# Kernel optimization log

Measured on AMD Instinct MI355X. Metric: run time of the kernel, lower is better.

The kernel has to match this reference:

```python
import jax, jax.numpy as jnp
import numpy as np

B, N, D = 2, 2048, 1024          # batch, query tokens, model dim
NC, DC = 77, 768                 # context tokens, context dim (CLIP)
H, DH = 16, 64                   # heads, head dim (H*DH == D)
FF = 4 * D                       # GEGLU inner dim
SCALE = DH ** -0.5
EPS = 1e-5


def setup_inputs() -> dict:
    key = jax.random.key(0)
    ks = iter(jax.random.split(key, 32))
    rn = lambda *s: jax.random.normal(next(ks), s, dtype=jnp.float32) * 0.02
    inp = {
        'x': jax.random.normal(next(ks), (B, N, D), dtype=jnp.float32),
        'context': jax.random.normal(next(ks), (B, NC, DC), dtype=jnp.float32),
        # attn1 (self-attention): all projections from dim D
        'w1_q': rn(D, D), 'w1_k': rn(D, D), 'w1_v': rn(D, D),
        'w1_o': rn(D, D), 'b1_o': jnp.zeros((D,), jnp.float32),
        # attn2 (cross-attention): k/v from context dim DC
        'w2_q': rn(D, D), 'w2_k': rn(DC, D), 'w2_v': rn(DC, D),
        'w2_o': rn(D, D), 'b2_o': jnp.zeros((D,), jnp.float32),
        # layernorms
        'ln1_g': jnp.ones((D,), jnp.float32), 'ln1_b': jnp.zeros((D,), jnp.float32),
        'ln2_g': jnp.ones((D,), jnp.float32), 'ln2_b': jnp.zeros((D,), jnp.float32),
        'ln3_g': jnp.ones((D,), jnp.float32), 'ln3_b': jnp.zeros((D,), jnp.float32),
        # GEGLU feed-forward: proj -> 2*FF (value, gate), then FF -> D
        'ff_w1': rn(D, 2 * FF), 'ff_b1': jnp.zeros((2 * FF,), jnp.float32),
        'ff_w2': rn(FF, D), 'ff_b2': jnp.zeros((D,), jnp.float32),
    }
    return inp


def _layer_norm(x, g, b):
    mu = jnp.mean(x, axis=-1, keepdims=True)
    var = jnp.mean(jnp.square(x - mu), axis=-1, keepdims=True)
    return (x - mu) * jax.lax.rsqrt(var + EPS) * g + b


def _attention(xq, ctx, wq, wk, wv, wo, bo):
    b, n, _ = xq.shape
    m = ctx.shape[1]
    q = (xq @ wq).reshape(b, n, H, DH)
    k = (ctx @ wk).reshape(b, m, H, DH)
    v = (ctx @ wv).reshape(b, m, H, DH)
    sim = jnp.einsum('bihd,bjhd->bhij', q, k) * SCALE
    attn = jax.nn.softmax(sim, axis=-1)
    out = jnp.einsum('bhij,bjhd->bihd', attn, v).reshape(b, n, H * DH)
    return out @ wo + bo


def reference(x, context,
              w1_q, w1_k, w1_v, w1_o, b1_o,
              w2_q, w2_k, w2_v, w2_o, b2_o,
              ln1_g, ln1_b, ln2_g, ln2_b, ln3_g, ln3_b,
              ff_w1, ff_b1, ff_w2, ff_b2):
    # self-attention + residual
    h = _layer_norm(x, ln1_g, ln1_b)
    x = _attention(h, h, w1_q, w1_k, w1_v, w1_o, b1_o) + x
    # cross-attention + residual
    h = _layer_norm(x, ln2_g, ln2_b)
    x = _attention(h, context, w2_q, w2_k, w2_v, w2_o, b2_o) + x
    # GEGLU feed-forward + residual (torch F.gelu is exact erf)
    h = _layer_norm(x, ln3_g, ln3_b)
    p = h @ ff_w1 + ff_b1
    val, gate = p[..., :FF], p[..., FF:]
    x = (val * jax.nn.gelu(gate, approximate=False)) @ ff_w2 + ff_b2 + x
    return x
```

## Files before the change

kernel.cpp:

```cpp
#include <hip/hip_runtime.h>
#include <hip/hip_bf16.h>
#include <math.h>

#define B_    2
#define N_    2048
#define D_    1024
#define NC_   77
#define DC_   768
#define H_    16
#define DH_   64
#define FF_   4096
#define EPS_  1e-5f
#define SCALE_ 0.125f
#define NEG_BIG -1e30f

typedef __attribute__((ext_vector_type(8))) short short8;
typedef __attribute__((ext_vector_type(4))) float f32x4;
#define MFMA16(a, b, c) __builtin_amdgcn_mfma_f32_16x16x32_bf16(a, b, c, 0, 0, 0)

static __device__ __forceinline__ unsigned short f2bf_raw(float f) {
    union { float f; unsigned int i; } x; x.f = f;
    unsigned int r = x.i + 0x7fffu + ((x.i >> 16) & 1u);
    return (unsigned short)(r >> 16);
}

static __device__ __forceinline__ float erf_fast(float x) {
    const float ax = fabsf(x);
    const float t = __frcp_rn(fmaf(0.3275911f, ax, 1.0f));
    float p = fmaf(1.061405429f, t, -1.453152027f);
    p = fmaf(p, t, 1.421413741f);
    p = fmaf(p, t, -0.284496736f);
    p = fmaf(p, t, 0.254829592f);
    p = p * t;
    const float e = __expf(-ax * ax);
    float r = fmaf(-p, e, 1.0f);
    return copysignf(r, x);
}

static __device__ __forceinline__ void gload16(const void* g, void* l) {
    __builtin_amdgcn_global_load_lds(
        (const __attribute__((address_space(1))) void*)g,
        (__attribute__((address_space(3))) void*)l, 16, 0, 0);
}

__global__ __launch_bounds__(256) void wtrans_k(const float* __restrict__ src,
                                                unsigned short* __restrict__ dst,
                                                int K, int N) {
    __shared__ unsigned short t[64][68];
    const int k0 = blockIdx.y * 64, n0 = blockIdx.x * 64;
    const int rr = threadIdx.x >> 4;
    const int cc = (threadIdx.x & 15) * 4;
#pragma unroll
    for (int p = 0; p < 4; p++) {
        int k = rr + p * 16;
        float4 vd = *(const float4*)&src[(size_t)(k0 + k) * N + n0 + cc];
        t[k][cc + 0] = f2bf_raw(vd.x); t[k][cc + 1] = f2bf_raw(vd.y);
        t[k][cc + 2] = f2bf_raw(vd.z); t[k][cc + 3] = f2bf_raw(vd.w);
    }
    __syncthreads();
#pragma unroll
    for (int p = 0; p < 4; p++) {
        int n = rr + p * 16;
        ushort4 o;
        o.x = t[cc + 0][n]; o.y = t[cc + 1][n];
        o.z = t[cc + 2][n]; o.w = t[cc + 3][n];
        *(ushort4*)&dst[(size_t)(n0 + n) * K + k0 + cc] = o;
    }
}

struct WT6 { const float* s[6]; unsigned short* d[6]; };
__global__ __launch_bounds__(256) void wtrans6_k(WT6 p) {
    __shared__ unsigned short t[64][68];
    const float* __restrict__ src = p.s[blockIdx.z];
    unsigned short* __restrict__ dst = p.d[blockIdx.z];
    const int K = 1024, N = 1024;
    const int k0 = blockIdx.y * 64, n0 = blockIdx.x * 64;
    const int rr = threadIdx.x >> 4;
    const int cc = (threadIdx.x & 15) * 4;
#pragma unroll
    for (int pq = 0; pq < 4; pq++) {
        int k = rr + pq * 16;
        float4 vd = *(const float4*)&src[(size_t)(k0 + k) * N + n0 + cc];
        t[k][cc + 0] = f2bf_raw(vd.x); t[k][cc + 1] = f2bf_raw(vd.y);
        t[k][cc + 2] = f2bf_raw(vd.z); t[k][cc + 3] = f2bf_raw(vd.w);
    }
    __syncthreads();
#pragma unroll
    for (int pq = 0; pq < 4; pq++) {
        int n = rr + pq * 16;
        ushort4 o;
        o.x = t[cc + 0][n]; o.y = t[cc + 1][n];
        o.z = t[cc + 2][n]; o.w = t[cc + 3][n];
        *(ushort4*)&dst[(size_t)(n0 + n) * K + k0 + cc] = o;
    }
}

__global__ __launch_bounds__(256) void ln_k(const float* __restrict__ x,
                                            const float* __restrict__ g,
                                            const float* __restrict__ b,
                                            unsigned short* __restrict__ out) {
    int row = blockIdx.x;
    const float* xr = x + (size_t)row * D_;
    float v0[4]; float s = 0.f, sq = 0.f;
#pragma unroll
    for (int i = 0; i < 4; i++) {
        float t = xr[threadIdx.x + 256 * i];
        v0[i] = t; s += t; sq += t * t;
    }
#pragma unroll
    for (int off = 32; off; off >>= 1) {
        s  += __shfl_xor(s,  off);
        sq += __shfl_xor(sq, off);
    }
    __shared__ float rs[4], rq[4];
    int wave = threadIdx.x >> 6, lane = threadIdx.x & 63;
    if (lane == 0) { rs[wave] = s; rq[wave] = sq; }
    __syncthreads();
    s  = rs[0] + rs[1] + rs[2] + rs[3];
    sq = rq[0] + rq[1] + rq[2] + rq[3];
    float mu  = s * (1.f / D_);
    float var = sq * (1.f / D_) - mu * mu;
    float inv = rsqrtf(var + EPS_);
#pragma unroll
    for (int i = 0; i < 4; i++) {
        int c = threadIdx.x + 256 * i;
        out[(size_t)row * D_ + c] = f2bf_raw((v0[i] - mu) * inv * g[c] + b[c]);
    }
}

__global__ __launch_bounds__(256) void gemm_mfma_k(
        const unsigned short* __restrict__ A,
        const unsigned short* __restrict__ BT,
        const float* __restrict__ bias,
        const float* __restrict__ res,
        float* __restrict__ outf,
        unsigned short* __restrict__ oq,
        unsigned short* __restrict__ ok,
        unsigned short* __restrict__ ov,
        int M, int N, int K, int mode) {
    __shared__ unsigned short As[128 * 32];
    __shared__ unsigned short Bs[128 * 32];
    const int tid = threadIdx.x;
    const int w = tid >> 6, lane = tid & 63, quad = lane >> 4, l15 = lane & 15;
    const int wm = w >> 1, wn = w & 1;
    const int m0 = blockIdx.y * 128, n0 = blockIdx.x * 128;
    const int srow = lane >> 2;
    const int schunk = lane & 3;
    const int kswz = (schunk ^ (srow & 3)) * 8;
    const int rdsw = (quad ^ (l15 & 3)) * 8;

    const unsigned short* pA[2];
    const unsigned short* pB[2];
#pragma unroll
    for (int i = 0; i < 2; i++) {
        int r = (w * 2 + i) * 16;
        pA[i] = &A[(size_t)(m0 + r + srow) * K + kswz];
        pB[i] = &BT[(size_t)(n0 + r + srow) * K + kswz];
    }

    f32x4 acc[4][4] = {};
    for (int k0 = 0; k0 < K; k0 += 32) {
#pragma unroll
        for (int i = 0; i < 2; i++) {
            int r = (w * 2 + i) * 16;
            gload16(pA[i], &As[r * 32]);
            gload16(pB[i], &Bs[r * 32]);
            pA[i] += 32; pB[i] += 32;
        }
        __syncthreads();
        short8 af[4], bf[4];
#pragma unroll
        for (int i = 0; i < 4; i++) {
            af[i] = *(const short8*)&As[(wm * 64 + i * 16 + l15) * 32 + rdsw];
            bf[i] = *(const short8*)&Bs[(wn * 64 + i * 16 + l15) * 32 + rdsw];
        }
#pragma unroll
        for (int i = 0; i < 4; i++)
#pragma unroll
            for (int j = 0; j < 4; j++)
                acc[i][j] = MFMA16(af[i], bf[j], acc[i][j]);
        __syncthreads();
    }
#pragma unroll
    for (int i = 0; i < 4; i++) {
#pragma unroll
        for (int r = 0; r < 4; r++) {
            const int row = m0 + wm * 64 + i * 16 + quad * 4 + r;
#pragma unroll
            for (int j = 0; j < 4; j++) {
                const int col = n0 + wn * 64 + j * 16 + l15;
                float c = acc[i][j][r];
                if (mode == 0) {
                    int which = col >> 10, cc = col & 1023;
                    unsigned short* dst = which == 0 ? oq : (which == 1 ? ok : ov);
                    dst[(size_t)row * 1024 + cc] = f2bf_raw(which == 0 ? c * SCALE_ : c);
                } else {
                    outf[(size_t)row * N + col] =
                        c + bias[col] + res[(size_t)row * N + col];
                }
            }
        }
    }
}

__global__ __launch_bounds__(256) void gemm64_k(
        const unsigned short* __restrict__ A,
        const unsigned short* __restrict__ BT,
        const float* __restrict__ bias,
        const float* __restrict__ res,
        float* __restrict__ outf,
        unsigned short* __restrict__ outb,
        float scale,
        int M, int N, int K, int mode) {
    __shared__ unsigned short As[64 * 64];
    __shared__ unsigned short Bs[64 * 64];
    const int tid = threadIdx.x;
    const int w = tid >> 6, lane = tid & 63, quad = lane >> 4, l15 = lane & 15;
    const int wm = w >> 1, wn = w & 1;
    const int m0 = blockIdx.y * 64, n0 = blockIdx.x * 64;
    const int sr8 = lane >> 3;
    const int sc8 = lane & 7;

    const unsigned short* pA[2];
    const unsigned short* pB[2];
#pragma unroll
    for (int i = 0; i < 2; i++) {
        int row = w * 16 + i * 8 + sr8;
        int gch = sc8 ^ (row & 7);
        pA[i] = &A[(size_t)(m0 + row) * K + gch * 8];
        pB[i] = &BT[(size_t)(n0 + row) * K + gch * 8];
    }

    f32x4 acc[2][2] = {};
    for (int k0 = 0; k0 < K; k0 += 64) {
#pragma unroll
        for (int i = 0; i < 2; i++) {
            gload16(pA[i], &As[(w * 16 + i * 8) * 64]);
            gload16(pB[i], &Bs[(w * 16 + i * 8) * 64]);
            pA[i] += 64; pB[i] += 64;
        }
        __syncthreads();
        short8 af[2][2], bf[2][2];
#pragma unroll
        for (int ii = 0; ii < 2; ii++) {
            int ra = wm * 32 + ii * 16 + l15;
            int rb = wn * 32 + ii * 16 + l15;
#pragma unroll
            for (int kh = 0; kh < 2; kh++) {
                int ca = (kh * 4 + quad) ^ (ra & 7);
                int cb = (kh * 4 + quad) ^ (rb & 7);
                af[ii][kh] = *(const short8*)&As[ra * 64 + ca * 8];
                bf[ii][kh] = *(const short8*)&Bs[rb * 64 + cb * 8];
            }
        }
#pragma unroll
        for (int ii = 0; ii < 2; ii++)
#pragma unroll
            for (int jj = 0; jj < 2; jj++) {
                acc[ii][jj] = MFMA16(af[ii][0], bf[jj][0], acc[ii][jj]);
                acc[ii][jj] = MFMA16(af[ii][1], bf[jj][1], acc[ii][jj]);
            }
        __syncthreads();
    }
#pragma unroll
    for (int ii = 0; ii < 2; ii++) {
#pragma unroll
        for (int r = 0; r < 4; r++) {
            const int row = m0 + wm * 32 + ii * 16 + quad * 4 + r;
#pragma unroll
            for (int jj = 0; jj < 2; jj++) {
                const int col = n0 + wn * 32 + jj * 16 + l15;
                float c = acc[ii][jj][r];
                if (mode == 0) {
                    outb[(size_t)row * N + col] = f2bf_raw(c * scale);
                } else {
                    outf[(size_t)row * N + col] =
                        c + bias[col] + res[(size_t)row * N + col];
                }
            }
        }
    }
}

__global__ __launch_bounds__(256, 4) void geglu_mfma_k(
        const unsigned short* __restrict__ A,
        const unsigned short* __restrict__ BT,
        const float* __restrict__ bias,
        unsigned short* __restrict__ outg,
        int M, int K) {
    __shared__ unsigned short As[64 * 64];
    __shared__ unsigned short Bv[128 * 64];
    __shared__ unsigned short Bg[128 * 64];
    const int tid = threadIdx.x;
    const int w = tid >> 6, lane = tid & 63, quad = lane >> 4, l15 = lane & 15;
    const int m0 = blockIdx.y * 64, n0 = blockIdx.x * 128;
    const int sr8 = lane >> 3, sc8 = lane & 7;

    f32x4 accv[4][2] = {}, accg[4][2] = {};
    for (int k0 = 0; k0 < K; k0 += 64) {
#pragma unroll
        for (int i = 0; i < 2; i++) {
            int row = w * 16 + i * 8 + sr8;
            int gch = sc8 ^ (row & 7);
            gload16(&A[(size_t)(m0 + row) * K + k0 + gch * 8], &As[(w * 16 + i * 8) * 64]);
        }
#pragma unroll
        for (int i = 0; i < 4; i++) {
            int row = w * 32 + i * 8 + sr8;
            int gch = sc8 ^ (row & 7);
            gload16(&BT[(size_t)(n0 + row) * K + k0 + gch * 8], &Bv[(w * 32 + i * 8) * 64]);
            gload16(&BT[(size_t)(FF_ + n0 + row) * K + k0 + gch * 8], &Bg[(w * 32 + i * 8) * 64]);
        }
        __syncthreads();
        short8 af[4][2];
#pragma unroll
        for (int ii = 0; ii < 4; ii++) {
            int ra = ii * 16 + l15;
#pragma unroll
            for (int kh = 0; kh < 2; kh++) {
                int ca = (kh * 4 + quad) ^ (ra & 7);
                af[ii][kh] = *(const short8*)&As[ra * 64 + ca * 8];
            }
        }
#pragma unroll
        for (int jj = 0; jj < 2; jj++) {
            const int rb = w * 32 + jj * 16 + l15;
            const int c0 = (0 * 4 + quad) ^ (rb & 7);
            const int c1 = (1 * 4 + quad) ^ (rb & 7);
            const short8 bv0 = *(const short8*)&Bv[rb * 64 + c0 * 8];
            const short8 bv1 = *(const short8*)&Bv[rb * 64 + c1 * 8];
            const short8 bg0 = *(const short8*)&Bg[rb * 64 + c0 * 8];
            const short8 bg1 = *(const short8*)&Bg[rb * 64 + c1 * 8];
#pragma unroll
            for (int ii = 0; ii < 4; ii++) {
                accv[ii][jj] = MFMA16(af[ii][0], bv0, accv[ii][jj]);
                accv[ii][jj] = MFMA16(af[ii][1], bv1, accv[ii][jj]);
                accg[ii][jj] = MFMA16(af[ii][0], bg0, accg[ii][jj]);
                accg[ii][jj] = MFMA16(af[ii][1], bg1, accg[ii][jj]);
            }
        }
        __syncthreads();
    }
#pragma unroll
    for (int ii = 0; ii < 4; ii++) {
#pragma unroll
        for (int r = 0; r < 4; r++) {
            const int row = m0 + ii * 16 + quad * 4 + r;
#pragma unroll
            for (int jj = 0; jj < 2; jj++) {
                const int col = n0 + w * 32 + jj * 16 + l15;
                float vv = accv[ii][jj][r] + bias[col];
                float gg = accg[ii][jj][r] + bias[col + FF_];
                float ge = 0.5f * gg * (1.f + erf_fast(gg * 0.70710678118654752f));
                outg[(size_t)row * FF_ + col] = f2bf_raw(vv * ge);
            }
        }
    }
}

__global__ __launch_bounds__(256) void gemm_k(const float* __restrict__ A,
                                              const float* __restrict__ W,
                                              unsigned short* __restrict__ outb,
                                              int M, int N, int K) {
    __shared__ float As[16][64];
    __shared__ float Ws[16][64];
    const int tx = threadIdx.x & 15;
    const int ty = threadIdx.x >> 4;
    const int m0 = blockIdx.y * 64, n0 = blockIdx.x * 64;
    const int lm = threadIdx.x >> 2;
    const int lk = (threadIdx.x & 3) * 4;
    const int wr = threadIdx.x >> 4;
    const int wc = (threadIdx.x & 15) * 4;
    float acc[4][4] = {};
    for (int k0 = 0; k0 < K; k0 += 16) {
        float4 av = make_float4(0.f, 0.f, 0.f, 0.f);
        if (m0 + lm < M) av = *(const float4*)&A[(size_t)(m0 + lm) * K + k0 + lk];
        float4 wv = *(const float4*)&W[(size_t)(k0 + wr) * N + n0 + wc];
        As[lk + 0][lm] = av.x; As[lk + 1][lm] = av.y;
        As[lk + 2][lm] = av.z; As[lk + 3][lm] = av.w;
        *(float4*)&Ws[wr][wc] = wv;
        __syncthreads();
#pragma unroll
        for (int kk = 0; kk < 16; kk++) {
            float4 a = *(const float4*)&As[kk][ty * 4];
            float4 b = *(const float4*)&Ws[kk][tx * 4];
            float ar[4] = { a.x, a.y, a.z, a.w };
            float br[4] = { b.x, b.y, b.z, b.w };
#pragma unroll
            for (int i = 0; i < 4; i++)
#pragma unroll
                for (int j = 0; j < 4; j++)
                    acc[i][j] = fmaf(ar[i], br[j], acc[i][j]);
        }
        __syncthreads();
    }
#pragma unroll
    for (int i = 0; i < 4; i++) {
        int row = m0 + ty * 4 + i;
        if (row >= M) continue;
        ushort4 u;
        u.x = f2bf_raw(acc[i][0]); u.y = f2bf_raw(acc[i][1]);
        u.z = f2bf_raw(acc[i][2]); u.w = f2bf_raw(acc[i][3]);
        *(ushort4*)&outb[(size_t)row * N + n0 + tx * 4] = u;
    }
}

__global__ __launch_bounds__(256) void vtrans_k(const unsigned short* __restrict__ v,
                                                unsigned short* __restrict__ vT,
                                                int ntok, int tokrows, int npad) {
    __shared__ unsigned short tile[64][68];
    const int bh = blockIdx.x, b = bh >> 4, h = bh & 15;
    const int t0 = blockIdx.y * 64;
    const int tt = threadIdx.x >> 4;
    const int dg = (threadIdx.x & 15) * 4;
#pragma unroll
    for (int p = 0; p < 4; p++) {
        int tok = t0 + tt + 16 * p;
        ushort4 val = make_ushort4(0, 0, 0, 0);
        if (tok < ntok)
            val = *(const ushort4*)&v[((size_t)(b * tokrows + tok)) * D_ + h * DH_ + dg];
        *(ushort4*)&tile[tt + 16 * p][dg] = val;
    }
    __syncthreads();
#pragma unroll
    for (int p = 0; p < 4; p++) {
        int d = tt + 16 * p;
        ushort4 w;
        w.x = tile[dg + 0][d]; w.y = tile[dg + 1][d];
        w.z = tile[dg + 2][d]; w.w = tile[dg + 3][d];
        *(ushort4*)&vT[((size_t)(bh * 64 + d)) * npad + t0 + dg] = w;
    }
}

__global__ __launch_bounds__(256, 4) void flash2_k(
        const unsigned short* __restrict__ qb,
        const unsigned short* __restrict__ kb,
        const unsigned short* __restrict__ vT,
        unsigned short* __restrict__ o,
        int n_kv, int kv_rows, int npadv, int ntiles) {
    __shared__ unsigned short Ks[2][64 * 64];
    __shared__ unsigned short Vs[2][64 * 64];
    __shared__ unsigned short Pls[4][16 * 64];
    const int bh = blockIdx.x, b = bh >> 4, h = bh & 15;
    const int w = threadIdx.x >> 6;
    const int lane = threadIdx.x & 63, quad = lane >> 4, l15 = lane & 15;
    const int q0 = blockIdx.y * 64 + w * 16;

    const size_t qoff = ((size_t)(b * N_ + q0 + l15)) * D_ + h * DH_ + quad * 8;
    const short8 qf0 = *(const short8*)&qb[qoff];
    const short8 qf1 = *(const short8*)&qb[qoff + 32];

    short8 onesf;
#pragma unroll
    for (int i = 0; i < 8; i++) onesf[i] = (short)0x3F80;

    const int sr = lane >> 3;
    const int sc = lane & 7;
    const unsigned short* vbase = vT + (size_t)(bh * 64) * npadv;

    auto stage = [&](int buf, int t) {
        const int j0 = t * 64;
#pragma unroll
        for (int i = 0; i < 2; i++) {
            const int row = w * 16 + i * 8 + sr;
            const int gch = (sc ^ (row & 7)) * 8;
            gload16(&kb[(size_t)(b * kv_rows + j0 + row) * D_ + h * DH_ + gch],
                    &Ks[buf][(w * 16 + i * 8) * 64]);
            gload16(&vbase[(size_t)row * npadv + j0 + gch],
                    &Vs[buf][(w * 16 + i * 8) * 64]);
        }
    };

    f32x4 O0 = {0.f, 0.f, 0.f, 0.f}, O1 = O0, O2 = O0, O3 = O0, L4 = O0;

    stage(0, 0);
    __syncthreads();

    for (int t = 0; t < ntiles; t++) {
        const int cur = t & 1;
        if (t + 1 < ntiles) stage(cur ^ 1, t + 1);
        const int j0 = t * 64;

        f32x4 s[4];
        __builtin_amdgcn_s_setprio(1);
#pragma unroll
        for (int cb = 0; cb < 4; cb++) {
            const int ra = 16 * cb + l15;
            const int sw = ra & 7;
            const short8 k0 = *(const short8*)&Ks[cur][ra * 64 + ((quad ^ sw) * 8)];
            const short8 k1 = *(const short8*)&Ks[cur][ra * 64 + (((quad + 4) ^ sw) * 8)];
            f32x4 z = {0.f, 0.f, 0.f, 0.f};
            z = MFMA16(qf0, k0, z);
            z = MFMA16(qf1, k1, z);
            s[cb] = z;
        }
        __builtin_amdgcn_s_setprio(0);
        if (j0 + 64 > n_kv) {
#pragma unroll
            for (int cb = 0; cb < 4; cb++)
                if (j0 + 16 * cb + l15 >= n_kv) {
                    s[cb][0] = NEG_BIG; s[cb][1] = NEG_BIG;
                    s[cb][2] = NEG_BIG; s[cb][3] = NEG_BIG;
                }
        }

#pragma unroll
        for (int cb = 0; cb < 4; cb++) {
            const int lc = (l15 >> 3) + 2 * cb;
            const int e = l15 & 7;
#pragma unroll
            for (int r = 0; r < 4; r++) {
                const int pr = quad * 4 + r;
                Pls[w][pr * 64 + ((lc ^ (pr & 7)) * 8 + e)] =
                    f2bf_raw(__expf(s[cb][r]));
            }
        }
        const int psw = l15 & 7;
        const short8 pf0 = *(const short8*)&Pls[w][l15 * 64 + ((quad ^ psw) * 8)];
        const short8 pf1 = *(const short8*)&Pls[w][l15 * 64 + (((quad + 4) ^ psw) * 8)];

        short8 vf[4][2];
#pragma unroll
        for (int n = 0; n < 4; n++) {
            const int rv = 16 * n + l15;
            const int vw = rv & 7;
            vf[n][0] = *(const short8*)&Vs[cur][rv * 64 + ((quad ^ vw) * 8)];
            vf[n][1] = *(const short8*)&Vs[cur][rv * 64 + (((quad + 4) ^ vw) * 8)];
        }
        __builtin_amdgcn_s_setprio(1);
        O0 = MFMA16(pf0, vf[0][0], O0); O0 = MFMA16(pf1, vf[0][1], O0);
        O1 = MFMA16(pf0, vf[1][0], O1); O1 = MFMA16(pf1, vf[1][1], O1);
        O2 = MFMA16(pf0, vf[2][0], O2); O2 = MFMA16(pf1, vf[2][1], O2);
        O3 = MFMA16(pf0, vf[3][0], O3); O3 = MFMA16(pf1, vf[3][1], O3);
        L4 = MFMA16(pf0, onesf, L4);    L4 = MFMA16(pf1, onesf, L4);
        __builtin_amdgcn_s_setprio(0);

        __syncthreads();
    }

    const size_t obase = ((size_t)(b * N_ + q0 + quad * 4)) * D_ + h * DH_ + l15;
#pragma unroll
    for (int r = 0; r < 4; r++) {
        const float inv = 1.0f / L4[r];
        unsigned short* orow = &o[obase + (size_t)r * D_];
        orow[0]  = f2bf_raw(O0[r] * inv);
        orow[16] = f2bf_raw(O1[r] * inv);
        orow[32] = f2bf_raw(O2[r] * inv);
        orow[48] = f2bf_raw(O3[r] * inv);
    }
}

extern "C" void kernel_launch(void* const* d_in, const int* in_sizes, int n_in,
                              void* d_out, int out_size, void* d_ws, size_t ws_size,
                              hipStream_t stream) {
    const float* x_in  = (const float*)d_in[0];
    const float* ctx_in= (const float*)d_in[1];
    const float* w1q = (const float*)d_in[2];
    const float* w1k = (const float*)d_in[3];
    const float* w1v = (const float*)d_in[4];
    const float* w1o = (const float*)d_in[5];
    const float* b1o = (const float*)d_in[6];
    const float* w2q = (const float*)d_in[7];
    const float* w2k = (const float*)d_in[8];
    const float* w2v = (const float*)d_in[9];
    const float* w2o = (const float*)d_in[10];
    const float* b2o = (const float*)d_in[11];
    const float* ln1g= (const float*)d_in[12];
    const float* ln1b= (const float*)d_in[13];
    const float* ln2g= (const float*)d_in[14];
    const float* ln2b= (const float*)d_in[15];
    const float* ln3g= (const float*)d_in[16];
    const float* ln3b= (const float*)d_in[17];
    const float* ffw1= (const float*)d_in[18];
    const float* ffb1= (const float*)d_in[19];
    const float* ffw2= (const float*)d_in[20];
    const float* ffb2= (const float*)d_in[21];
    float* out_f = (float*)d_out;

    char* ws = (char*)d_ws;
    unsigned short* wqkvT = (unsigned short*)(ws);
    unsigned short* w1oT  = (unsigned short*)(ws + (size_t)( 6 << 20));
    unsigned short* w2qT  = (unsigned short*)(ws + (size_t)( 8 << 20));
    unsigned short* w2oT  = (unsigned short*)(ws + (size_t)(10 << 20));
    unsigned short* ffw1T = (unsigned short*)(ws + (size_t)(12 << 20));
    unsigned short* ffw2T = (unsigned short*)(ws + (size_t)(28 << 20));
    float*          xbuf  = (float*)         (ws + (size_t)(36 << 20));
    unsigned short* h     = (unsigned short*)(ws + (size_t)(52 << 20));
    unsigned short* qb    = (unsigned short*)(ws + (size_t)(60 << 20));
    unsigned short* kb    = (unsigned short*)(ws + (size_t)(68 << 20));
    unsigned short* vTb   = (unsigned short*)(ws + (size_t)(76 << 20));
    unsigned short* vb    = (unsigned short*)(ws + (size_t)(84 << 20));
    unsigned short* g     = (unsigned short*)(ws + (size_t)(60 << 20));

    const int MT = B_ * N_;

    auto wt = [&](const float* src, unsigned short* dst, int K, int N) {
        hipLaunchKernelGGL(wtrans_k, dim3(N / 64, K / 64), dim3(256), 0, stream, src, dst, K, N);
    };
    auto gmm = [&](const unsigned short* A, const unsigned short* BT,
                   const float* bias, const float* res, float* outf,
                   unsigned short* oq, unsigned short* ok, unsigned short* ov,
                   int M, int N, int K, int mode) {
        hipLaunchKernelGGL(gemm_mfma_k, dim3(N / 128, M / 128), dim3(256), 0, stream,
                           A, BT, bias, res, outf, oq, ok, ov, M, N, K, mode);
    };
    auto g64 = [&](const unsigned short* A, const unsigned short* BT,
                   const float* bias, const float* res, float* outf,
                   unsigned short* outb, float scale, int M, int N, int K, int mode) {
        hipLaunchKernelGGL(gemm64_k, dim3(N / 64, M / 64), dim3(256), 0, stream,
                           A, BT, bias, res, outf, outb, scale, M, N, K, mode);
    };

    WT6 wt6;
    wt6.s[0] = w1q; wt6.d[0] = wqkvT;
    wt6.s[1] = w1k; wt6.d[1] = wqkvT + (1024 * 1024);
    wt6.s[2] = w1v; wt6.d[2] = wqkvT + (2048 * 1024);
    wt6.s[3] = w1o; wt6.d[3] = w1oT;
    wt6.s[4] = w2q; wt6.d[4] = w2qT;
    wt6.s[5] = w2o; wt6.d[5] = w2oT;
    hipLaunchKernelGGL(wtrans6_k, dim3(16, 16, 6), dim3(256), 0, stream, wt6);
    wt(ffw1, ffw1T, D_, 2 * FF_);
    wt(ffw2, ffw2T, FF_, D_);

    hipLaunchKernelGGL(ln_k, dim3(MT), dim3(256), 0, stream, x_in, ln1g, ln1b, h);
    gmm(h, wqkvT, nullptr, nullptr, nullptr, qb, kb, vb, MT, 3072, D_, 0);
    hipLaunchKernelGGL(vtrans_k, dim3(B_ * H_, N_ / 64), dim3(256), 0, stream,
                       vb, vTb, N_, N_, N_);
    hipLaunchKernelGGL(flash2_k, dim3(B_ * H_, N_ / 64), dim3(256), 0, stream,
                       qb, kb, vTb, vb , N_, N_, N_, N_ / 64);
    g64(vb , w1oT, b1o, x_in, xbuf, nullptr, 1.0f, MT, D_, D_, 1);

    hipLaunchKernelGGL(ln_k, dim3(MT), dim3(256), 0, stream, xbuf, ln2g, ln2b, h);
    g64(h, w2qT, nullptr, nullptr, nullptr, qb, SCALE_, MT, D_, D_, 0);
    hipLaunchKernelGGL(gemm_k, dim3(D_ / 64, 3), dim3(256), 0, stream,
                       ctx_in, w2k, kb, B_ * NC_, D_, DC_);
    hipLaunchKernelGGL(gemm_k, dim3(D_ / 64, 3), dim3(256), 0, stream,
                       ctx_in, w2v, vb, B_ * NC_, D_, DC_);
    hipLaunchKernelGGL(vtrans_k, dim3(B_ * H_, 2), dim3(256), 0, stream,
                       vb, vTb, NC_, NC_, 128);
    hipLaunchKernelGGL(flash2_k, dim3(B_ * H_, N_ / 64), dim3(256), 0, stream,
                       qb, kb, vTb, vb , NC_, NC_, 128, 2);
    g64(vb , w2oT, b2o, xbuf, xbuf, nullptr, 1.0f, MT, D_, D_, 1);

    hipLaunchKernelGGL(ln_k, dim3(MT), dim3(256), 0, stream, xbuf, ln3g, ln3b, h);
    hipLaunchKernelGGL(geglu_mfma_k, dim3(FF_ / 128, MT / 64), dim3(256), 0, stream,
                       h, ffw1T, ffb1, g, MT, D_);
    g64(g, ffw2T, ffb2, xbuf, out_f, nullptr, 1.0f, MT, D_, FF_, 1);
}
```

Before: 611.2 us.

## Replace both GEMM kernels with a single 64x128-tile wave-column GEMM

Merges the 128x128 K=32 QKV GEMM and the 64x64 K=64 projection GEMM into one kernel with a 64x128 tile and K-step of 64. Each wave owns a 32-column strip and reuses A fragments across all four row tiles, and launch bounds request 4 blocks per CU. This gives the 1024-wide projection and FF2 GEMMs larger tiles with more operand reuse and fewer blocks, and gives the QKV GEMM a deeper K step. The cost is fewer blocks for the D-wide GEMMs and a different register/LDS footprint.

```diff
diff --git a/kernel.cpp b/kernel.cpp
--- a/kernel.cpp
+++ b/kernel.cpp
@@ -128,7 +128,7 @@
     }
 }
 
-__global__ __launch_bounds__(256) void gemm_mfma_k(
+__global__ __launch_bounds__(256, 4) void gemmw_k(
         const unsigned short* __restrict__ A,
         const unsigned short* __restrict__ BT,
         const float* __restrict__ bias,
@@ -137,142 +137,70 @@
         unsigned short* __restrict__ oq,
         unsigned short* __restrict__ ok,
         unsigned short* __restrict__ ov,
+        float scale,
         int M, int N, int K, int mode) {
-    __shared__ unsigned short As[128 * 32];
-    __shared__ unsigned short Bs[128 * 32];
+    __shared__ unsigned short As[64 * 64];
+    __shared__ unsigned short Bs[128 * 64];
     const int tid = threadIdx.x;
     const int w = tid >> 6, lane = tid & 63, quad = lane >> 4, l15 = lane & 15;
-    const int wm = w >> 1, wn = w & 1;
-    const int m0 = blockIdx.y * 128, n0 = blockIdx.x * 128;
-    const int srow = lane >> 2;
-    const int schunk = lane & 3;
-    const int kswz = (schunk ^ (srow & 3)) * 8;
-    const int rdsw = (quad ^ (l15 & 3)) * 8;
-
-    const unsigned short* pA[2];
-    const unsigned short* pB[2];
-#pragma unroll
-    for (int i = 0; i < 2; i++) {
-        int r = (w * 2 + i) * 16;
-        pA[i] = &A[(size_t)(m0 + r + srow) * K + kswz];
-        pB[i] = &BT[(size_t)(n0 + r + srow) * K + kswz];
-    }
-
-    f32x4 acc[4][4] = {};
-    for (int k0 = 0; k0 < K; k0 += 32) {
+    const int m0 = blockIdx.y * 64, n0 = blockIdx.x * 128;
+    const int sr8 = lane >> 3, sc8 = lane & 7;
+
+    f32x4 acc[4][2] = {};
+    for (int k0 = 0; k0 < K; k0 += 64) {
 #pragma unroll
         for (int i = 0; i < 2; i++) {
-            int r = (w * 2 + i) * 16;
-            gload16(pA[i], &As[r * 32]);
-            gload16(pB[i], &Bs[r * 32]);
-            pA[i] += 32; pB[i] += 32;
-        }
-        __syncthreads();
-        short8 af[4], bf[4];
+            int row = w * 16 + i * 8 + sr8;
+            int gch = sc8 ^ (row & 7);
+            gload16(&A[(size_t)(m0 + row) * K + k0 + gch * 8], &As[(w * 16 + i * 8) * 64]);
+        }
 #pragma unroll
         for (int i = 0; i < 4; i++) {
-            af[i] = *(const short8*)&As[(wm * 64 + i * 16 + l15) * 32 + rdsw];
-            bf[i] = *(const short8*)&Bs[(wn * 64 + i * 16 + l15) * 32 + rdsw];
-        }
-#pragma unroll
-        for (int i = 0; i < 4; i++)
-#pragma unroll
-            for (int j = 0; j < 4; j++)
-                acc[i][j] = MFMA16(af[i], bf[j], acc[i][j]);
-        __syncthreads();
-    }
-#pragma unroll
-    for (int i = 0; i < 4; i++) {
+            int row = w * 32 + i * 8 + sr8;
+            int gch = sc8 ^ (row & 7);
+            gload16(&BT[(size_t)(n0 + row) * K + k0 + gch * 8], &Bs[(w * 32 + i * 8) * 64]);
+        }
+        __syncthreads();
+        short8 af[4][2];
+#pragma unroll
+        for (int ii = 0; ii < 4; ii++) {
+            int ra = ii * 16 + l15;
+#pragma unroll
+            for (int kh = 0; kh < 2; kh++) {
+                int ca = (kh * 4 + quad) ^ (ra & 7);
+                af[ii][kh] = *(const short8*)&As[ra * 64 + ca * 8];
+            }
+        }
+#pragma unroll
+        for (int jj = 0; jj < 2; jj++) {
+            const int rb = w * 32 + jj * 16 + l15;
+            const int c0 = (0 * 4 + quad) ^ (rb & 7);
+            const int c1 = (1 * 4 + quad) ^ (rb & 7);
+            const short8 b0 = *(const short8*)&Bs[rb * 64 + c0 * 8];
+            const short8 b1 = *(const short8*)&Bs[rb * 64 + c1 * 8];
+#pragma unroll
+            for (int ii = 0; ii < 4; ii++) {
+                acc[ii][jj] = MFMA16(af[ii][0], b0, acc[ii][jj]);
+                acc[ii][jj] = MFMA16(af[ii][1], b1, acc[ii][jj]);
+            }
+        }
+        __syncthreads();
+    }
+#pragma unroll
+    for (int ii = 0; ii < 4; ii++) {
 #pragma unroll
         for (int r = 0; r < 4; r++) {
-            const int row = m0 + wm * 64 + i * 16 + quad * 4 + r;
-#pragma unroll
-            for (int j = 0; j < 4; j++) {
-                const int col = n0 + wn * 64 + j * 16 + l15;
-                float c = acc[i][j][r];
+            const int row = m0 + ii * 16 + quad * 4 + r;
+#pragma unroll
+            for (int jj = 0; jj < 2; jj++) {
+                const int col = n0 + w * 32 + jj * 16 + l15;
+                float c = acc[ii][jj][r];
                 if (mode == 0) {
                     int which = col >> 10, cc = col & 1023;
                     unsigned short* dst = which == 0 ? oq : (which == 1 ? ok : ov);
-                    dst[(size_t)row * 1024 + cc] = f2bf_raw(which == 0 ? c * SCALE_ : c);
-                } else {
-                    outf[(size_t)row * N + col] =
-                        c + bias[col] + res[(size_t)row * N + col];
-                }
-            }
-        }
-    }
-}
-
-__global__ __launch_bounds__(256) void gemm64_k(
-        const unsigned short* __restrict__ A,
-        const unsigned short* __restrict__ BT,
-        const float* __restrict__ bias,
-        const float* __restrict__ res,
-        float* __restrict__ outf,
-        unsigned short* __restrict__ outb,
-        float scale,
-        int M, int N, int K, int mode) {
-    __shared__ unsigned short As[64 * 64];
-    __shared__ unsigned short Bs[64 * 64];
-    const int tid = threadIdx.x;
-    const int w = tid >> 6, lane = tid & 63, quad = lane >> 4, l15 = lane & 15;
-    const int wm = w >> 1, wn = w & 1;
-    const int m0 = blockIdx.y * 64, n0 = blockIdx.x * 64;
-    const int sr8 = lane >> 3;
-    const int sc8 = lane & 7;
-
-    const unsigned short* pA[2];
-    const unsigned short* pB[2];
-#pragma unroll
-    for (int i = 0; i < 2; i++) {
-        int row = w * 16 + i * 8 + sr8;
-        int gch = sc8 ^ (row & 7);
-        pA[i] = &A[(size_t)(m0 + row) * K + gch * 8];
-        pB[i] = &BT[(size_t)(n0 + row) * K + gch * 8];
-    }
-
-    f32x4 acc[2][2] = {};
-    for (int k0 = 0; k0 < K; k0 += 64) {
-#pragma unroll
-        for (int i = 0; i < 2; i++) {
-            gload16(pA[i], &As[(w * 16 + i * 8) * 64]);
-            gload16(pB[i], &Bs[(w * 16 + i * 8) * 64]);
-            pA[i] += 64; pB[i] += 64;
-        }
-        __syncthreads();
-        short8 af[2][2], bf[2][2];
-#pragma unroll
-        for (int ii = 0; ii < 2; ii++) {
-            int ra = wm * 32 + ii * 16 + l15;
-            int rb = wn * 32 + ii * 16 + l15;
-#pragma unroll
-            for (int kh = 0; kh < 2; kh++) {
-                int ca = (kh * 4 + quad) ^ (ra & 7);
-                int cb = (kh * 4 + quad) ^ (rb & 7);
-                af[ii][kh] = *(const short8*)&As[ra * 64 + ca * 8];
-                bf[ii][kh] = *(const short8*)&Bs[rb * 64 + cb * 8];
-            }
-        }
-#pragma unroll
-        for (int ii = 0; ii < 2; ii++)
-#pragma unroll
-            for (int jj = 0; jj < 2; jj++) {
-                acc[ii][jj] = MFMA16(af[ii][0], bf[jj][0], acc[ii][jj]);
-                acc[ii][jj] = MFMA16(af[ii][1], bf[jj][1], acc[ii][jj]);
-            }
-        __syncthreads();
-    }
-#pragma unroll
-    for (int ii = 0; ii < 2; ii++) {
-#pragma unroll
-        for (int r = 0; r < 4; r++) {
-            const int row = m0 + wm * 32 + ii * 16 + quad * 4 + r;
-#pragma unroll
-            for (int jj = 0; jj < 2; jj++) {
-                const int col = n0 + wn * 32 + jj * 16 + l15;
-                float c = acc[ii][jj][r];
-                if (mode == 0) {
-                    outb[(size_t)row * N + col] = f2bf_raw(c * scale);
+                    dst[(size_t)row * 1024 + cc] = f2bf_raw(which == 0 ? c * scale : c);
+                } else if (mode == 2) {
+                    oq[(size_t)row * N + col] = f2bf_raw(c * scale);
                 } else {
                     outf[(size_t)row * N + col] =
                         c + bias[col] + res[(size_t)row * N + col];
@@ -597,18 +525,12 @@
     auto wt = [&](const float* src, unsigned short* dst, int K, int N) {
         hipLaunchKernelGGL(wtrans_k, dim3(N / 64, K / 64), dim3(256), 0, stream, src, dst, K, N);
     };
-    auto gmm = [&](const unsigned short* A, const unsigned short* BT,
-                   const float* bias, const float* res, float* outf,
-                   unsigned short* oq, unsigned short* ok, unsigned short* ov,
-                   int M, int N, int K, int mode) {
-        hipLaunchKernelGGL(gemm_mfma_k, dim3(N / 128, M / 128), dim3(256), 0, stream,
-                           A, BT, bias, res, outf, oq, ok, ov, M, N, K, mode);
-    };
-    auto g64 = [&](const unsigned short* A, const unsigned short* BT,
-                   const float* bias, const float* res, float* outf,
-                   unsigned short* outb, float scale, int M, int N, int K, int mode) {
-        hipLaunchKernelGGL(gemm64_k, dim3(N / 64, M / 64), dim3(256), 0, stream,
-                           A, BT, bias, res, outf, outb, scale, M, N, K, mode);
+    auto gw = [&](const unsigned short* A, const unsigned short* BT,
+                  const float* bias, const float* res, float* outf,
+                  unsigned short* oq, unsigned short* ok, unsigned short* ov,
+                  float scale, int M, int N, int K, int mode) {
+        hipLaunchKernelGGL(gemmw_k, dim3(N / 128, M / 64), dim3(256), 0, stream,
+                           A, BT, bias, res, outf, oq, ok, ov, scale, M, N, K, mode);
     };
 
     WT6 wt6;
@@ -623,15 +545,17 @@
     wt(ffw2, ffw2T, FF_, D_);
 
     hipLaunchKernelGGL(ln_k, dim3(MT), dim3(256), 0, stream, x_in, ln1g, ln1b, h);
-    gmm(h, wqkvT, nullptr, nullptr, nullptr, qb, kb, vb, MT, 3072, D_, 0);
+    gw(h, wqkvT, nullptr, nullptr, nullptr, qb, kb, vb, SCALE_, MT, 3072, D_, 0);
     hipLaunchKernelGGL(vtrans_k, dim3(B_ * H_, N_ / 64), dim3(256), 0, stream,
                        vb, vTb, N_, N_, N_);
     hipLaunchKernelGGL(flash2_k, dim3(B_ * H_, N_ / 64), dim3(256), 0, stream,
                        qb, kb, vTb, vb , N_, N_, N_, N_ / 64);
-    g64(vb , w1oT, b1o, x_in, xbuf, nullptr, 1.0f, MT, D_, D_, 1);
+    gw(vb , w1oT, b1o, x_in, xbuf, nullptr, nullptr, nullptr,
+       1.0f, MT, D_, D_, 1);
 
     hipLaunchKernelGGL(ln_k, dim3(MT), dim3(256), 0, stream, xbuf, ln2g, ln2b, h);
-    g64(h, w2qT, nullptr, nullptr, nullptr, qb, SCALE_, MT, D_, D_, 0);
+    gw(h, w2qT, nullptr, nullptr, nullptr, qb, nullptr, nullptr,
+       SCALE_, MT, D_, D_, 2);
     hipLaunchKernelGGL(gemm_k, dim3(D_ / 64, 3), dim3(256), 0, stream,
                        ctx_in, w2k, kb, B_ * NC_, D_, DC_);
     hipLaunchKernelGGL(gemm_k, dim3(D_ / 64, 3), dim3(256), 0, stream,
@@ -640,10 +564,12 @@
                        vb, vTb, NC_, NC_, 128);
     hipLaunchKernelGGL(flash2_k, dim3(B_ * H_, N_ / 64), dim3(256), 0, stream,
                        qb, kb, vTb, vb , NC_, NC_, 128, 2);
-    g64(vb , w2oT, b2o, xbuf, xbuf, nullptr, 1.0f, MT, D_, D_, 1);
+    gw(vb , w2oT, b2o, xbuf, xbuf, nullptr, nullptr, nullptr,
+       1.0f, MT, D_, D_, 1);
 
     hipLaunchKernelGGL(ln_k, dim3(MT), dim3(256), 0, stream, xbuf, ln3g, ln3b, h);
     hipLaunchKernelGGL(geglu_mfma_k, dim3(FF_ / 128, MT / 64), dim3(256), 0, stream,
                        h, ffw1T, ffb1, g, MT, D_);
-    g64(g, ffw2T, ffb2, xbuf, out_f, nullptr, 1.0f, MT, D_, FF_, 1);
-}
+    gw(g, ffw2T, ffb2, xbuf, out_f, nullptr, nullptr, nullptr,
+       1.0f, MT, D_, FF_, 1);
+}
```

New measurement: 611.1 us. About the same (-0.0%).
